# Kernel optimization log

Measured on AMD Instinct MI355X. Metric: run time of the kernel, lower is better.

The kernel has to match this reference:

```python
import jax, jax.numpy as jnp
import numpy as np

B, S, H, D = 256, 512, 512, 1  # batch, seq_len, rnn_hid_size (== S*D), input_dim


def lstm_cell(x, h, c, Wih, Whh, bih, bhh):
    # torch.nn.LSTMCell: gates ordered i, f, g, o
    g = x @ Wih.T + bih + h @ Whh.T + bhh  # [B, 4H]
    i, f, gg, o = jnp.split(g, 4, axis=-1)
    i = jax.nn.sigmoid(i)
    f = jax.nn.sigmoid(f)
    gg = jnp.tanh(gg)
    o = jax.nn.sigmoid(o)
    c_new = f * c + i * gg
    h_new = o * jnp.tanh(c_new)
    return h_new, c_new


def setup_inputs() -> dict:
    key = jax.random.key(0)
    ks = jax.random.split(key, 14)
    sc = 1.0 / np.sqrt(H)  # torch LSTMCell/Linear default uniform bound
    u = lambda k, shape: jax.random.uniform(k, shape, jnp.float32, -sc, sc)
    values = jax.random.normal(ks[0], (B, S), jnp.float32)
    masks = jax.random.randint(ks[1], (B, S), 0, 2).astype(jnp.float32)
    return {
        "values": values,
        "masks": masks,
        "Wih_f": u(ks[2], (4 * H, D)), "Whh_f": u(ks[3], (4 * H, H)),
        "bih_f": u(ks[4], (4 * H,)), "bhh_f": u(ks[5], (4 * H,)),
        "Wih_b": u(ks[6], (4 * H, D)), "Whh_b": u(ks[7], (4 * H, H)),
        "bih_b": u(ks[8], (4 * H,)), "bhh_b": u(ks[9], (4 * H,)),
        "W_imp": u(ks[10], (D, H)), "b_imp": u(ks[11], (D,)),
    }


def reference(values, masks, Wih_f, Whh_f, bih_f, bhh_f,
              Wih_b, Whh_b, bih_b, bhh_b, W_imp, b_imp):
    x_f = values[:, :, None]  # [B, S, 1]
    m_f = masks[:, :, None]
    # flip over axis 2 (size 1) is a no-op, matching the original exactly
    x_b = jnp.flip(x_f, axis=2)
    m_b = jnp.flip(m_f, axis=2)

    start_f = jnp.full((B, D), 128.0, jnp.float32)
    start_b = jnp.full((B, D), -128.0, jnp.float32)
    z = jnp.zeros((B, H), jnp.float32)
    h_f, c_f = lstm_cell(start_f, z, z, Wih_f, Whh_f, bih_f, bhh_f)
    h_b, c_b = lstm_cell(start_b, z, z, Wih_b, Whh_b, bih_b, bhh_b)

    xs = (jnp.swapaxes(x_f, 0, 1), jnp.swapaxes(m_f, 0, 1),
          jnp.swapaxes(x_b, 0, 1), jnp.swapaxes(m_b, 0, 1))  # [S, B, 1] each

    def step(carry, inp):
        hf, cf, hb, cb = carry
        xf, mf, xb, mb = inp
        imp_f = hf @ W_imp.T + b_imp
        imp_b = hb @ W_imp.T + b_imp
        cc_f = (1.0 - mf) * xf + mf * imp_f
        cc_b = (1.0 - mb) * xb + mb * imp_b
        hf, cf = lstm_cell(cc_f, hf, cf, Wih_f, Whh_f, bih_f, bhh_f)
        hb, cb = lstm_cell(cc_b, hb, cb, Wih_b, Whh_b, bih_b, bhh_b)
        return (hf, cf, hb, cb), None

    (h_f, c_f, h_b, c_b), _ = jax.lax.scan(step, (h_f, c_f, h_b, c_b), xs)
    h = h_f + h_b  # [B, H]
    imputations = h.reshape(B, S, D)  # requires H == S * D
    out = imputations * (1.0 - m_f) + x_f * m_f
    return h, out
```

## Files before the change

kernel.cpp:

```cpp
#include <hip/hip_runtime.h>
#include <stdint.h>

#define B_ 256
#define S_ 512
#define H_ 512

#define XM_STRIDE 513
#define LDS_BYTES 56320

typedef __attribute__((ext_vector_type(4))) float f32x4;
typedef __attribute__((ext_vector_type(4))) int   i32x4;
typedef __attribute__((ext_vector_type(8))) short s16x8;

__device__ __forceinline__ short f2bf(float f) {
    union { float f; uint32_t u; } c; c.f = f;
    uint32_t u = c.u;
    u += 0x7fffu + ((u >> 16) & 1u);
    return (short)(u >> 16);
}
__device__ __forceinline__ float bflo(uint32_t u) { return __builtin_bit_cast(float, u << 16); }
__device__ __forceinline__ float bfhi(uint32_t u) { return __builtin_bit_cast(float, u & 0xffff0000u); }
__device__ __forceinline__ float sig_(float x)  { return 1.0f / (1.0f + __expf(-x)); }
__device__ __forceinline__ float tanh_(float x) { return 1.0f - 2.0f / (1.0f + __expf(2.0f * x)); }

__device__ __forceinline__ void load_a16_issue(const void* p, i32x4* a) {
    asm volatile(
        "global_load_dwordx4 %0, %16, off sc0 sc1\n\t"
        "global_load_dwordx4 %1, %16, off offset:64 sc0 sc1\n\t"
        "global_load_dwordx4 %2, %16, off offset:128 sc0 sc1\n\t"
        "global_load_dwordx4 %3, %16, off offset:192 sc0 sc1\n\t"
        "global_load_dwordx4 %4, %16, off offset:256 sc0 sc1\n\t"
        "global_load_dwordx4 %5, %16, off offset:320 sc0 sc1\n\t"
        "global_load_dwordx4 %6, %16, off offset:384 sc0 sc1\n\t"
        "global_load_dwordx4 %7, %16, off offset:448 sc0 sc1\n\t"
        "global_load_dwordx4 %8, %16, off offset:512 sc0 sc1\n\t"
        "global_load_dwordx4 %9, %16, off offset:576 sc0 sc1\n\t"
        "global_load_dwordx4 %10, %16, off offset:640 sc0 sc1\n\t"
        "global_load_dwordx4 %11, %16, off offset:704 sc0 sc1\n\t"
        "global_load_dwordx4 %12, %16, off offset:768 sc0 sc1\n\t"
        "global_load_dwordx4 %13, %16, off offset:832 sc0 sc1\n\t"
        "global_load_dwordx4 %14, %16, off offset:896 sc0 sc1\n\t"
        "global_load_dwordx4 %15, %16, off offset:960 sc0 sc1"
        : "=v"(a[0]), "=v"(a[1]), "=v"(a[2]), "=v"(a[3]),
          "=v"(a[4]), "=v"(a[5]), "=v"(a[6]), "=v"(a[7]),
          "=v"(a[8]), "=v"(a[9]), "=v"(a[10]), "=v"(a[11]),
          "=v"(a[12]), "=v"(a[13]), "=v"(a[14]), "=v"(a[15])
        : "v"(p)
        : "memory");
}
#define AWAIT(imm, x0, x1, x2, x3) \
    asm volatile("s_waitcnt vmcnt(" #imm ")" : "+v"(x0), "+v"(x1), "+v"(x2), "+v"(x3) :: "memory")

__device__ __forceinline__ void store_h4(void* p, int h0, int h1, int h2, int h3) {
    asm volatile(
        "global_store_short %4, %0, off sc0 sc1\n\t"
        "global_store_short %4, %1, off offset:1024 sc0 sc1\n\t"
        "global_store_short %4, %2, off offset:2048 sc0 sc1\n\t"
        "global_store_short %4, %3, off offset:3072 sc0 sc1"
        :: "v"(h0), "v"(h1), "v"(h2), "v"(h3), "v"(p)
        : "memory");
}

__global__ void __launch_bounds__(128, 1)
lstm_kernel(const float* __restrict__ values, const float* __restrict__ masks,
            const float* __restrict__ Wih_f, const float* __restrict__ Whh_f,
            const float* __restrict__ bih_f, const float* __restrict__ bhh_f,
            const float* __restrict__ Wih_b, const float* __restrict__ Whh_b,
            const float* __restrict__ bih_b, const float* __restrict__ bhh_b,
            const float* __restrict__ W_imp, const float* __restrict__ b_imp,
            unsigned int* ctrs, short* h_buf, float* hfin)
{
    extern __shared__ char smem_raw[];
    short*    imp_lds = (short*)smem_raw;
    uint32_t* xm_lds  = (uint32_t*)(smem_raw + 16384);

    uint32_t* flags = (uint32_t*)ctrs + 64;

    const int tid  = threadIdx.x;
    const int lane = tid & 63;
    const int wave = tid >> 6;
    const int nw = wave;

    const int bid = blockIdx.x;
    const int g   = bid & 15;
    const int w   = (bid >> 4) & 15;
    const int d   = bid >> 8;
    const int cluster = d * 16 + g;

    const float* Whh = d ? Whh_b : Whh_f;
    const float* Wih = d ? Wih_b : Wih_f;
    const float* bih = d ? bih_b : bih_f;
    const float* bhh = d ? bhh_b : bhh_f;

    const int col16 = lane & 15;
    const int koff4 = lane >> 4;
    const int jcol  = w * 32 + nw * 16 + col16;

    for (int c = tid; c < 1024; c += 128) {
        int ckoff = (c >> 4) & 3, ckb = c >> 6;
        int k0 = ckb * 32 + ckoff * 8;
        short* dst = &imp_lds[c * 8];
        #pragma unroll
        for (int j = 0; j < 8; ++j) dst[j] = f2bf(W_imp[k0 + j]);
    }
    for (int i = tid; i < 16 * 512; i += 128) {
        int r = i >> 9, s = i & 511;
        float x = values[(g * 16 + r) * S_ + s];
        float m = masks[(g * 16 + r) * S_ + s];
        float a = x * (1.0f - m);
        xm_lds[r * XM_STRIDE + s] =
            (uint32_t)(uint16_t)f2bf(a) | ((uint32_t)(uint16_t)f2bf(m) << 16);
    }

    s16x8 bfr[4][16];
    {
        const float* base = Whh + (size_t)jcol * 512 + koff4 * 8;
        #pragma unroll
        for (int gg = 0; gg < 4; ++gg) {
            const float* src = base + (size_t)gg * 512 * 512;
            #pragma unroll
            for (int kb = 0; kb < 16; ++kb) {
                f32x4 v0 = *(const f32x4*)(src + kb * 32);
                f32x4 v1 = *(const f32x4*)(src + kb * 32 + 4);
                s16x8 b;
                b[0] = f2bf(v0[0]); b[1] = f2bf(v0[1]); b[2] = f2bf(v0[2]); b[3] = f2bf(v0[3]);
                b[4] = f2bf(v1[0]); b[5] = f2bf(v1[1]); b[6] = f2bf(v1[2]); b[7] = f2bf(v1[3]);
                bfr[gg][kb] = b;
            }
        }
    }

    float bias[4], wih[4];
    #pragma unroll
    for (int gg = 0; gg < 4; ++gg) {
        int gc = gg * 512 + jcol;
        bias[gg] = bih[gc] + bhh[gc];
        wih[gg]  = Wih[gc];
    }
    const float bimp  = b_imp[0];
    const float start = d ? -128.0f : 128.0f;

    const int arow    = g * 16 + col16;
    const int rowloc  = koff4 * 4;
    const int rowbase = g * 16 + rowloc;
    const int imp_off = (koff4 * 16 + col16) * 8;

    uint32_t*       myflag = flags + cluster * 16 + w;
    const uint32_t* pollp  = flags + cluster * 16 + col16;

    __syncthreads();

    float c_reg[4];
    {
        float pre[4];
        #pragma unroll
        for (int gg = 0; gg < 4; ++gg) pre[gg] = start * wih[gg] + bias[gg];
        float i0 = sig_(pre[0]), g0 = tanh_(pre[2]), o0 = sig_(pre[3]);
        float c0 = i0 * g0;
        float h0 = o0 * tanh_(c0);
        #pragma unroll
        for (int r = 0; r < 4; ++r) c_reg[r] = c0;
        int hb16 = (int)(unsigned short)(unsigned)f2bf(h0);
        short* dst = h_buf + d * (B_ * H_) + (size_t)rowbase * H_ + jcol;
        store_h4(dst, hb16, hb16, hb16, hb16);
    }
    asm volatile("s_waitcnt vmcnt(0)" ::: "memory");
    __syncthreads();
    if (tid == 0)
        asm volatile("global_store_dword %0, %1, off sc0 sc1" :: "v"(myflag), "v"(1u) : "memory");

    for (int t = 0; t < S_; ++t) {
        const int p = t & 1;
        const short* hb_r = h_buf + p       * (2 * B_ * H_) + d * (B_ * H_);
        short*       hb_w = h_buf + (p ^ 1) * (2 * B_ * H_) + d * (B_ * H_);

        if (wave == 0) {
            const uint32_t tgt = (uint32_t)(t + 1);
            for (;;) {
                uint32_t f;
                asm volatile("global_load_dword %0, %1, off sc0 sc1\n\ts_waitcnt vmcnt(0)"
                             : "=v"(f) : "v"(pollp) : "memory");
                if (__ballot(f >= tgt) == ~0ull) break;
                __builtin_amdgcn_s_sleep(2);
            }
        }
        __syncthreads();

        i32x4 a_regs[16];
        load_a16_issue(hb_r + (size_t)arow * H_ + koff4 * 8, a_regs);

        f32x4 acc0 = {0,0,0,0}, acc1 = {0,0,0,0}, acc2 = {0,0,0,0}, acc3 = {0,0,0,0};
        f32x4 acc4 = {0,0,0,0};
        AWAIT(12, a_regs[0], a_regs[1], a_regs[2], a_regs[3]);
        #pragma unroll
        for (int kb = 0; kb < 4; ++kb) {
            s16x8 a = __builtin_bit_cast(s16x8, a_regs[kb]);
            acc0 = __builtin_amdgcn_mfma_f32_16x16x32_bf16(a, bfr[0][kb], acc0, 0, 0, 0);
            acc1 = __builtin_amdgcn_mfma_f32_16x16x32_bf16(a, bfr[1][kb], acc1, 0, 0, 0);
            acc2 = __builtin_amdgcn_mfma_f32_16x16x32_bf16(a, bfr[2][kb], acc2, 0, 0, 0);
            acc3 = __builtin_amdgcn_mfma_f32_16x16x32_bf16(a, bfr[3][kb], acc3, 0, 0, 0);
            s16x8 b4 = *(const s16x8*)&imp_lds[kb * 512 + imp_off];
            acc4 = __builtin_amdgcn_mfma_f32_16x16x32_bf16(a, b4, acc4, 0, 0, 0);
        }
        AWAIT(8, a_regs[4], a_regs[5], a_regs[6], a_regs[7]);
        #pragma unroll
        for (int kb = 4; kb < 8; ++kb) {
            s16x8 a = __builtin_bit_cast(s16x8, a_regs[kb]);
            acc0 = __builtin_amdgcn_mfma_f32_16x16x32_bf16(a, bfr[0][kb], acc0, 0, 0, 0);
            acc1 = __builtin_amdgcn_mfma_f32_16x16x32_bf16(a, bfr[1][kb], acc1, 0, 0, 0);
            acc2 = __builtin_amdgcn_mfma_f32_16x16x32_bf16(a, bfr[2][kb], acc2, 0, 0, 0);
            acc3 = __builtin_amdgcn_mfma_f32_16x16x32_bf16(a, bfr[3][kb], acc3, 0, 0, 0);
            s16x8 b4 = *(const s16x8*)&imp_lds[kb * 512 + imp_off];
            acc4 = __builtin_amdgcn_mfma_f32_16x16x32_bf16(a, b4, acc4, 0, 0, 0);
        }
        AWAIT(4, a_regs[8], a_regs[9], a_regs[10], a_regs[11]);
        #pragma unroll
        for (int kb = 8; kb < 12; ++kb) {
            s16x8 a = __builtin_bit_cast(s16x8, a_regs[kb]);
            acc0 = __builtin_amdgcn_mfma_f32_16x16x32_bf16(a, bfr[0][kb], acc0, 0, 0, 0);
            acc1 = __builtin_amdgcn_mfma_f32_16x16x32_bf16(a, bfr[1][kb], acc1, 0, 0, 0);
            acc2 = __builtin_amdgcn_mfma_f32_16x16x32_bf16(a, bfr[2][kb], acc2, 0, 0, 0);
            acc3 = __builtin_amdgcn_mfma_f32_16x16x32_bf16(a, bfr[3][kb], acc3, 0, 0, 0);
            s16x8 b4 = *(const s16x8*)&imp_lds[kb * 512 + imp_off];
            acc4 = __builtin_amdgcn_mfma_f32_16x16x32_bf16(a, b4, acc4, 0, 0, 0);
        }
        AWAIT(0, a_regs[12], a_regs[13], a_regs[14], a_regs[15]);
        #pragma unroll
        for (int kb = 12; kb < 16; ++kb) {
            s16x8 a = __builtin_bit_cast(s16x8, a_regs[kb]);
            acc0 = __builtin_amdgcn_mfma_f32_16x16x32_bf16(a, bfr[0][kb], acc0, 0, 0, 0);
            acc1 = __builtin_amdgcn_mfma_f32_16x16x32_bf16(a, bfr[1][kb], acc1, 0, 0, 0);
            acc2 = __builtin_amdgcn_mfma_f32_16x16x32_bf16(a, bfr[2][kb], acc2, 0, 0, 0);
            acc3 = __builtin_amdgcn_mfma_f32_16x16x32_bf16(a, bfr[3][kb], acc3, 0, 0, 0);
            s16x8 b4 = *(const s16x8*)&imp_lds[kb * 512 + imp_off];
            acc4 = __builtin_amdgcn_mfma_f32_16x16x32_bf16(a, b4, acc4, 0, 0, 0);
        }

        int hbits[4];
        #pragma unroll
        for (int r = 0; r < 4; ++r) {
            uint32_t pk = xm_lds[(rowloc + r) * XM_STRIDE + t];
            float cc = bflo(pk) + bfhi(pk) * (acc4[r] + bimp);
            float pi = acc0[r] + cc * wih[0] + bias[0];
            float pf = acc1[r] + cc * wih[1] + bias[1];
            float pg = acc2[r] + cc * wih[2] + bias[2];
            float po = acc3[r] + cc * wih[3] + bias[3];
            float iv = sig_(pi), fv = sig_(pf), gv = tanh_(pg), ov = sig_(po);
            c_reg[r] = fv * c_reg[r] + iv * gv;
            float hn = ov * tanh_(c_reg[r]);
            hbits[r] = (int)(unsigned short)(unsigned)f2bf(hn);
            if (t == S_ - 1) hfin[d * (B_ * H_) + (rowbase + r) * H_ + jcol] = hn;
        }
        store_h4(hb_w + (size_t)rowbase * H_ + jcol, hbits[0], hbits[1], hbits[2], hbits[3]);

        asm volatile("s_waitcnt vmcnt(0)" ::: "memory");
        __syncthreads();
        if (tid == 0)
            asm volatile("global_store_dword %0, %1, off sc0 sc1"
                         :: "v"(myflag), "v"((uint32_t)(t + 2)) : "memory");
    }
}

__global__ void __launch_bounds__(256)
epilogue_kernel(const float* __restrict__ values, const float* __restrict__ masks,
                const float* __restrict__ hfin, float* __restrict__ out)
{
    int i = blockIdx.x * 256 + threadIdx.x;
    float h = hfin[i] + hfin[B_ * H_ + i];
    out[i] = h;
    float xv = values[i], mv = masks[i];
    out[B_ * H_ + i] = h * (1.0f - mv) + xv * mv;
}

extern "C" void kernel_launch(void* const* d_in, const int* in_sizes, int n_in,
                              void* d_out, int out_size, void* d_ws, size_t ws_size,
                              hipStream_t stream) {
    const float* values = (const float*)d_in[0];
    const float* masks  = (const float*)d_in[1];
    const float* Wih_f  = (const float*)d_in[2];
    const float* Whh_f  = (const float*)d_in[3];
    const float* bih_f  = (const float*)d_in[4];
    const float* bhh_f  = (const float*)d_in[5];
    const float* Wih_b  = (const float*)d_in[6];
    const float* Whh_b  = (const float*)d_in[7];
    const float* bih_b  = (const float*)d_in[8];
    const float* bhh_b  = (const float*)d_in[9];
    const float* W_imp  = (const float*)d_in[10];
    const float* b_imp  = (const float*)d_in[11];

    unsigned int* ctrs = (unsigned int*)d_ws;
    short* h_buf = (short*)((char*)d_ws + 8192);
    float* hfin  = (float*)((char*)d_ws + 8192 + 2 * 2 * B_ * H_ * sizeof(short));

    hipMemsetAsync(d_ws, 0, 8192, stream);

    hipFuncSetAttribute((const void*)lstm_kernel,
                        hipFuncAttributeMaxDynamicSharedMemorySize, LDS_BYTES);

    void* args[] = {
        (void*)&values, (void*)&masks,
        (void*)&Wih_f, (void*)&Whh_f, (void*)&bih_f, (void*)&bhh_f,
        (void*)&Wih_b, (void*)&Whh_b, (void*)&bih_b, (void*)&bhh_b,
        (void*)&W_imp, (void*)&b_imp,
        (void*)&ctrs, (void*)&h_buf, (void*)&hfin
    };
    hipError_t err = hipLaunchCooperativeKernel((const void*)lstm_kernel,
                                                dim3(512), dim3(128), args,
                                                (unsigned int)LDS_BYTES, stream);
    if (err != hipSuccess) {
        lstm_kernel<<<dim3(512), dim3(128), LDS_BYTES, stream>>>(
            values, masks, Wih_f, Whh_f, bih_f, bhh_f,
            Wih_b, Whh_b, bih_b, bhh_b, W_imp, b_imp, ctrs, h_buf, hfin);
    }

    epilogue_kernel<<<dim3((B_ * H_) / 256), dim3(256), 0, stream>>>(
        values, masks, hfin, (float*)d_out);
}
```

Before: 2.342 ms.

## Replace flag-based barrier with step-tagged h values, widen blocks to 256 threads

Drops the per-cluster flag counters. Each bf16 h value is now packed into a 32-bit word with the timestep in its upper half, and readers spin on the data itself until every tag matches, so the separate flag store, its vmcnt wait and the extra syncthreads per step are gone. Blocks grow to four waves covering 64 columns, and the grid halves to 256 blocks. Each wave loads a quarter of the h row slice and shares it through a swizzled LDS buffer before the MFMAs. The cost is twice the h_buf traffic, a larger memset of the workspace, and hfin now being written into the output buffer before the epilogue reads it back.

```diff
diff --git a/kernel.cpp b/kernel.cpp
--- a/kernel.cpp
+++ b/kernel.cpp
@@ -6,7 +6,7 @@
 #define H_ 512
 
 #define XM_STRIDE 513
-#define LDS_BYTES 56320
+#define LDS_BYTES 81984
 
 typedef __attribute__((ext_vector_type(4))) float f32x4;
 typedef __attribute__((ext_vector_type(4))) int   i32x4;
@@ -23,69 +23,63 @@
 __device__ __forceinline__ float sig_(float x)  { return 1.0f / (1.0f + __expf(-x)); }
 __device__ __forceinline__ float tanh_(float x) { return 1.0f - 2.0f / (1.0f + __expf(2.0f * x)); }
 
-__device__ __forceinline__ void load_a16_issue(const void* p, i32x4* a) {
+__device__ __forceinline__ uint32_t pklo(uint32_t hi, uint32_t lo) {
+    return __builtin_amdgcn_perm(hi, lo, 0x05040100u);
+}
+
+__device__ __forceinline__ void load_a8_issue(const void* p, i32x4* a) {
     asm volatile(
-        "global_load_dwordx4 %0, %16, off sc0 sc1\n\t"
-        "global_load_dwordx4 %1, %16, off offset:64 sc0 sc1\n\t"
-        "global_load_dwordx4 %2, %16, off offset:128 sc0 sc1\n\t"
-        "global_load_dwordx4 %3, %16, off offset:192 sc0 sc1\n\t"
-        "global_load_dwordx4 %4, %16, off offset:256 sc0 sc1\n\t"
-        "global_load_dwordx4 %5, %16, off offset:320 sc0 sc1\n\t"
-        "global_load_dwordx4 %6, %16, off offset:384 sc0 sc1\n\t"
-        "global_load_dwordx4 %7, %16, off offset:448 sc0 sc1\n\t"
-        "global_load_dwordx4 %8, %16, off offset:512 sc0 sc1\n\t"
-        "global_load_dwordx4 %9, %16, off offset:576 sc0 sc1\n\t"
-        "global_load_dwordx4 %10, %16, off offset:640 sc0 sc1\n\t"
-        "global_load_dwordx4 %11, %16, off offset:704 sc0 sc1\n\t"
-        "global_load_dwordx4 %12, %16, off offset:768 sc0 sc1\n\t"
-        "global_load_dwordx4 %13, %16, off offset:832 sc0 sc1\n\t"
-        "global_load_dwordx4 %14, %16, off offset:896 sc0 sc1\n\t"
-        "global_load_dwordx4 %15, %16, off offset:960 sc0 sc1"
-        : "=v"(a[0]), "=v"(a[1]), "=v"(a[2]), "=v"(a[3]),
-          "=v"(a[4]), "=v"(a[5]), "=v"(a[6]), "=v"(a[7]),
-          "=v"(a[8]), "=v"(a[9]), "=v"(a[10]), "=v"(a[11]),
-          "=v"(a[12]), "=v"(a[13]), "=v"(a[14]), "=v"(a[15])
+        "global_load_dwordx4 %0, %8, off sc0 sc1\n\t"
+        "global_load_dwordx4 %1, %8, off offset:16 sc0 sc1\n\t"
+        "global_load_dwordx4 %2, %8, off offset:128 sc0 sc1\n\t"
+        "global_load_dwordx4 %3, %8, off offset:144 sc0 sc1\n\t"
+        "global_load_dwordx4 %4, %8, off offset:256 sc0 sc1\n\t"
+        "global_load_dwordx4 %5, %8, off offset:272 sc0 sc1\n\t"
+        "global_load_dwordx4 %6, %8, off offset:384 sc0 sc1\n\t"
+        "global_load_dwordx4 %7, %8, off offset:400 sc0 sc1"
+        : "=&v"(a[0]), "=&v"(a[1]), "=&v"(a[2]), "=&v"(a[3]),
+          "=&v"(a[4]), "=&v"(a[5]), "=&v"(a[6]), "=&v"(a[7])
         : "v"(p)
         : "memory");
 }
-#define AWAIT(imm, x0, x1, x2, x3) \
-    asm volatile("s_waitcnt vmcnt(" #imm ")" : "+v"(x0), "+v"(x1), "+v"(x2), "+v"(x3) :: "memory")
-
-__device__ __forceinline__ void store_h4(void* p, int h0, int h1, int h2, int h3) {
+#define AWAIT8(a) \
+    asm volatile("s_waitcnt vmcnt(0)" \
+        : "+v"(a[0]), "+v"(a[1]), "+v"(a[2]), "+v"(a[3]), \
+          "+v"(a[4]), "+v"(a[5]), "+v"(a[6]), "+v"(a[7]) :: "memory")
+
+__device__ __forceinline__ void store_h4d(void* p, uint32_t d0, uint32_t d1,
+                                          uint32_t d2, uint32_t d3) {
     asm volatile(
-        "global_store_short %4, %0, off sc0 sc1\n\t"
-        "global_store_short %4, %1, off offset:1024 sc0 sc1\n\t"
-        "global_store_short %4, %2, off offset:2048 sc0 sc1\n\t"
-        "global_store_short %4, %3, off offset:3072 sc0 sc1"
-        :: "v"(h0), "v"(h1), "v"(h2), "v"(h3), "v"(p)
+        "global_store_dword %4, %0, off offset:-4096 sc0 sc1\n\t"
+        "global_store_dword %4, %1, off offset:-2048 sc0 sc1\n\t"
+        "global_store_dword %4, %2, off sc0 sc1\n\t"
+        "global_store_dword %4, %3, off offset:2048 sc0 sc1"
+        :: "v"(d0), "v"(d1), "v"(d2), "v"(d3), "v"(p)
         : "memory");
 }
 
-__global__ void __launch_bounds__(128, 1)
+__global__ void __launch_bounds__(256, 1)
 lstm_kernel(const float* __restrict__ values, const float* __restrict__ masks,
             const float* __restrict__ Wih_f, const float* __restrict__ Whh_f,
             const float* __restrict__ bih_f, const float* __restrict__ bhh_f,
             const float* __restrict__ Wih_b, const float* __restrict__ Whh_b,
             const float* __restrict__ bih_b, const float* __restrict__ bhh_b,
             const float* __restrict__ W_imp, const float* __restrict__ b_imp,
-            unsigned int* ctrs, short* h_buf, float* hfin)
+            uint32_t* h_buf, float* hfin)
 {
     extern __shared__ char smem_raw[];
     short*    imp_lds = (short*)smem_raw;
     uint32_t* xm_lds  = (uint32_t*)(smem_raw + 16384);
-
-    uint32_t* flags = (uint32_t*)ctrs + 64;
+    char*     aP      = smem_raw + 49216;
 
     const int tid  = threadIdx.x;
     const int lane = tid & 63;
-    const int wave = tid >> 6;
-    const int nw = wave;
+    const int nw   = tid >> 6;
 
     const int bid = blockIdx.x;
     const int g   = bid & 15;
-    const int w   = (bid >> 4) & 15;
-    const int d   = bid >> 8;
-    const int cluster = d * 16 + g;
+    const int w   = (bid >> 4) & 7;
+    const int d   = bid >> 7;
 
     const float* Whh = d ? Whh_b : Whh_f;
     const float* Wih = d ? Wih_b : Wih_f;
@@ -94,16 +88,17 @@
 
     const int col16 = lane & 15;
     const int koff4 = lane >> 4;
-    const int jcol  = w * 32 + nw * 16 + col16;
-
-    for (int c = tid; c < 1024; c += 128) {
+    const int jcol  = w * 64 + nw * 16 + col16;
+    const int swz   = (col16 & 7) << 4;
+
+    for (int c = tid; c < 1024; c += 256) {
         int ckoff = (c >> 4) & 3, ckb = c >> 6;
         int k0 = ckb * 32 + ckoff * 8;
         short* dst = &imp_lds[c * 8];
         #pragma unroll
         for (int j = 0; j < 8; ++j) dst[j] = f2bf(W_imp[k0 + j]);
     }
-    for (int i = tid; i < 16 * 512; i += 128) {
+    for (int i = tid; i < 16 * 512; i += 256) {
         int r = i >> 9, s = i & 511;
         float x = values[(g * 16 + r) * S_ + s];
         float m = masks[(g * 16 + r) * S_ + s];
@@ -145,11 +140,6 @@
     const int rowbase = g * 16 + rowloc;
     const int imp_off = (koff4 * 16 + col16) * 8;
 
-    uint32_t*       myflag = flags + cluster * 16 + w;
-    const uint32_t* pollp  = flags + cluster * 16 + col16;
-
-    __syncthreads();
-
     float c_reg[4];
     {
         float pre[4];
@@ -160,41 +150,61 @@
         float h0 = o0 * tanh_(c0);
         #pragma unroll
         for (int r = 0; r < 4; ++r) c_reg[r] = c0;
-        int hb16 = (int)(unsigned short)(unsigned)f2bf(h0);
-        short* dst = h_buf + d * (B_ * H_) + (size_t)rowbase * H_ + jcol;
-        store_h4(dst, hb16, hb16, hb16, hb16);
-    }
-    asm volatile("s_waitcnt vmcnt(0)" ::: "memory");
+        uint32_t dwi = (1u << 16) | (uint32_t)(unsigned short)(unsigned)f2bf(h0);
+        uint32_t* dst = h_buf + (size_t)d * (B_ * H_)
+                        + (size_t)(rowbase + 2) * H_ + jcol;
+        store_h4d(dst, dwi, dwi, dwi, dwi);
+    }
+
     __syncthreads();
-    if (tid == 0)
-        asm volatile("global_store_dword %0, %1, off sc0 sc1" :: "v"(myflag), "v"(1u) : "memory");
 
     for (int t = 0; t < S_; ++t) {
         const int p = t & 1;
-        const short* hb_r = h_buf + p       * (2 * B_ * H_) + d * (B_ * H_);
-        short*       hb_w = h_buf + (p ^ 1) * (2 * B_ * H_) + d * (B_ * H_);
-
-        if (wave == 0) {
-            const uint32_t tgt = (uint32_t)(t + 1);
-            for (;;) {
-                uint32_t f;
-                asm volatile("global_load_dword %0, %1, off sc0 sc1\n\ts_waitcnt vmcnt(0)"
-                             : "=v"(f) : "v"(pollp) : "memory");
-                if (__ballot(f >= tgt) == ~0ull) break;
-                __builtin_amdgcn_s_sleep(2);
+        const uint32_t* hb_r = h_buf + (size_t)p       * (2 * B_ * H_) + (size_t)d * (B_ * H_);
+        uint32_t*       hb_w = h_buf + (size_t)(p ^ 1) * (2 * B_ * H_) + (size_t)d * (B_ * H_);
+
+        const uint32_t tgtv = (uint32_t)(t + 1) << 16;
+        const uint32_t* ap = hb_r + (size_t)arow * H_ + nw * 128 + koff4 * 8;
+        i32x4 araw[8];
+        load_a8_issue(ap, araw);
+        for (;;) {
+            AWAIT8(araw);
+            uint32_t mn = 0xffffffffu;
+            #pragma unroll
+            for (int j = 0; j < 8; ++j) {
+                uint32_t u0 = (uint32_t)araw[j][0], u1 = (uint32_t)araw[j][1];
+                uint32_t u2 = (uint32_t)araw[j][2], u3 = (uint32_t)araw[j][3];
+                uint32_t m0 = u0 < u1 ? u0 : u1;
+                uint32_t m1 = u2 < u3 ? u2 : u3;
+                uint32_t mm = m0 < m1 ? m0 : m1;
+                mn = mn < mm ? mn : mm;
             }
+            if (__ballot(mn >= tgtv) == ~0ull) break;
+            __builtin_amdgcn_s_sleep(2);
+            load_a8_issue(ap, araw);
+        }
+
+        {
+            char* wb = aP + p * 16384 + col16 * 1024;
+            #pragma unroll
+            for (int j = 0; j < 4; ++j) {
+                i32x4 pk;
+                pk[0] = (int)pklo((uint32_t)araw[2*j  ][1], (uint32_t)araw[2*j  ][0]);
+                pk[1] = (int)pklo((uint32_t)araw[2*j  ][3], (uint32_t)araw[2*j  ][2]);
+                pk[2] = (int)pklo((uint32_t)araw[2*j+1][1], (uint32_t)araw[2*j+1][0]);
+                pk[3] = (int)pklo((uint32_t)araw[2*j+1][3], (uint32_t)araw[2*j+1][2]);
+                int boff = (((nw * 4 + j) * 64 + koff4 * 16) ^ swz);
+                *(i32x4*)(wb + boff) = pk;
+            }
         }
         __syncthreads();
-
-        i32x4 a_regs[16];
-        load_a16_issue(hb_r + (size_t)arow * H_ + koff4 * 8, a_regs);
 
         f32x4 acc0 = {0,0,0,0}, acc1 = {0,0,0,0}, acc2 = {0,0,0,0}, acc3 = {0,0,0,0};
         f32x4 acc4 = {0,0,0,0};
-        AWAIT(12, a_regs[0], a_regs[1], a_regs[2], a_regs[3]);
-        #pragma unroll
-        for (int kb = 0; kb < 4; ++kb) {
-            s16x8 a = __builtin_bit_cast(s16x8, a_regs[kb]);
+        const char* rb = aP + p * 16384 + col16 * 1024;
+        #pragma unroll
+        for (int kb = 0; kb < 16; ++kb) {
+            s16x8 a = *(const s16x8*)(rb + ((kb * 64 + koff4 * 16) ^ swz));
             acc0 = __builtin_amdgcn_mfma_f32_16x16x32_bf16(a, bfr[0][kb], acc0, 0, 0, 0);
             acc1 = __builtin_amdgcn_mfma_f32_16x16x32_bf16(a, bfr[1][kb], acc1, 0, 0, 0);
             acc2 = __builtin_amdgcn_mfma_f32_16x16x32_bf16(a, bfr[2][kb], acc2, 0, 0, 0);
@@ -202,41 +212,9 @@
             s16x8 b4 = *(const s16x8*)&imp_lds[kb * 512 + imp_off];
             acc4 = __builtin_amdgcn_mfma_f32_16x16x32_bf16(a, b4, acc4, 0, 0, 0);
         }
-        AWAIT(8, a_regs[4], a_regs[5], a_regs[6], a_regs[7]);
-        #pragma unroll
-        for (int kb = 4; kb < 8; ++kb) {
-            s16x8 a = __builtin_bit_cast(s16x8, a_regs[kb]);
-            acc0 = __builtin_amdgcn_mfma_f32_16x16x32_bf16(a, bfr[0][kb], acc0, 0, 0, 0);
-            acc1 = __builtin_amdgcn_mfma_f32_16x16x32_bf16(a, bfr[1][kb], acc1, 0, 0, 0);
-            acc2 = __builtin_amdgcn_mfma_f32_16x16x32_bf16(a, bfr[2][kb], acc2, 0, 0, 0);
-            acc3 = __builtin_amdgcn_mfma_f32_16x16x32_bf16(a, bfr[3][kb], acc3, 0, 0, 0);
-            s16x8 b4 = *(const s16x8*)&imp_lds[kb * 512 + imp_off];
-            acc4 = __builtin_amdgcn_mfma_f32_16x16x32_bf16(a, b4, acc4, 0, 0, 0);
-        }
-        AWAIT(4, a_regs[8], a_regs[9], a_regs[10], a_regs[11]);
-        #pragma unroll
-        for (int kb = 8; kb < 12; ++kb) {
-            s16x8 a = __builtin_bit_cast(s16x8, a_regs[kb]);
-            acc0 = __builtin_amdgcn_mfma_f32_16x16x32_bf16(a, bfr[0][kb], acc0, 0, 0, 0);
-            acc1 = __builtin_amdgcn_mfma_f32_16x16x32_bf16(a, bfr[1][kb], acc1, 0, 0, 0);
-            acc2 = __builtin_amdgcn_mfma_f32_16x16x32_bf16(a, bfr[2][kb], acc2, 0, 0, 0);
-            acc3 = __builtin_amdgcn_mfma_f32_16x16x32_bf16(a, bfr[3][kb], acc3, 0, 0, 0);
-            s16x8 b4 = *(const s16x8*)&imp_lds[kb * 512 + imp_off];
-            acc4 = __builtin_amdgcn_mfma_f32_16x16x32_bf16(a, b4, acc4, 0, 0, 0);
-        }
-        AWAIT(0, a_regs[12], a_regs[13], a_regs[14], a_regs[15]);
-        #pragma unroll
-        for (int kb = 12; kb < 16; ++kb) {
-            s16x8 a = __builtin_bit_cast(s16x8, a_regs[kb]);
-            acc0 = __builtin_amdgcn_mfma_f32_16x16x32_bf16(a, bfr[0][kb], acc0, 0, 0, 0);
-            acc1 = __builtin_amdgcn_mfma_f32_16x16x32_bf16(a, bfr[1][kb], acc1, 0, 0, 0);
-            acc2 = __builtin_amdgcn_mfma_f32_16x16x32_bf16(a, bfr[2][kb], acc2, 0, 0, 0);
-            acc3 = __builtin_amdgcn_mfma_f32_16x16x32_bf16(a, bfr[3][kb], acc3, 0, 0, 0);
-            s16x8 b4 = *(const s16x8*)&imp_lds[kb * 512 + imp_off];
-            acc4 = __builtin_amdgcn_mfma_f32_16x16x32_bf16(a, b4, acc4, 0, 0, 0);
-        }
-
-        int hbits[4];
+
+        const uint32_t tagw = (uint32_t)(t + 2) << 16;
+        uint32_t dw[4];
         #pragma unroll
         for (int r = 0; r < 4; ++r) {
             uint32_t pk = xm_lds[(rowloc + r) * XM_STRIDE + t];
@@ -248,16 +226,10 @@
             float iv = sig_(pi), fv = sig_(pf), gv = tanh_(pg), ov = sig_(po);
             c_reg[r] = fv * c_reg[r] + iv * gv;
             float hn = ov * tanh_(c_reg[r]);
-            hbits[r] = (int)(unsigned short)(unsigned)f2bf(hn);
+            dw[r] = tagw | (uint32_t)(unsigned short)(unsigned)f2bf(hn);
             if (t == S_ - 1) hfin[d * (B_ * H_) + (rowbase + r) * H_ + jcol] = hn;
         }
-        store_h4(hb_w + (size_t)rowbase * H_ + jcol, hbits[0], hbits[1], hbits[2], hbits[3]);
-
-        asm volatile("s_waitcnt vmcnt(0)" ::: "memory");
-        __syncthreads();
-        if (tid == 0)
-            asm volatile("global_store_dword %0, %1, off sc0 sc1"
-                         :: "v"(myflag), "v"((uint32_t)(t + 2)) : "memory");
+        store_h4d(hb_w + (size_t)(rowbase + 2) * H_ + jcol, dw[0], dw[1], dw[2], dw[3]);
     }
 }
 
@@ -267,9 +239,10 @@
 {
     int i = blockIdx.x * 256 + threadIdx.x;
     float h = hfin[i] + hfin[B_ * H_ + i];
+    float xv = values[i], mv = masks[i];
+    float blend = h * (1.0f - mv) + xv * mv;
     out[i] = h;
-    float xv = values[i], mv = masks[i];
-    out[B_ * H_ + i] = h * (1.0f - mv) + xv * mv;
+    out[B_ * H_ + i] = blend;
 }
 
 extern "C" void kernel_launch(void* const* d_in, const int* in_sizes, int n_in,
@@ -288,11 +261,10 @@
     const float* W_imp  = (const float*)d_in[10];
     const float* b_imp  = (const float*)d_in[11];
 
-    unsigned int* ctrs = (unsigned int*)d_ws;
-    short* h_buf = (short*)((char*)d_ws + 8192);
-    float* hfin  = (float*)((char*)d_ws + 8192 + 2 * 2 * B_ * H_ * sizeof(short));
-
-    hipMemsetAsync(d_ws, 0, 8192, stream);
+    uint32_t* h_buf = (uint32_t*)d_ws;
+    float*    hfin  = (float*)d_out;
+
+    hipMemsetAsync(d_ws, 0, (size_t)2 * 2 * B_ * H_ * 4, stream);
 
     hipFuncSetAttribute((const void*)lstm_kernel,
                         hipFuncAttributeMaxDynamicSharedMemorySize, LDS_BYTES);
@@ -302,15 +274,15 @@
         (void*)&Wih_f, (void*)&Whh_f, (void*)&bih_f, (void*)&bhh_f,
         (void*)&Wih_b, (void*)&Whh_b, (void*)&bih_b, (void*)&bhh_b,
         (void*)&W_imp, (void*)&b_imp,
-        (void*)&ctrs, (void*)&h_buf, (void*)&hfin
+        (void*)&h_buf, (void*)&hfin
     };
     hipError_t err = hipLaunchCooperativeKernel((const void*)lstm_kernel,
-                                                dim3(512), dim3(128), args,
+                                                dim3(256), dim3(256), args,
                                                 (unsigned int)LDS_BYTES, stream);
     if (err != hipSuccess) {
-        lstm_kernel<<<dim3(512), dim3(128), LDS_BYTES, stream>>>(
+        lstm_kernel<<<dim3(256), dim3(256), LDS_BYTES, stream>>>(
             values, masks, Wih_f, Whh_f, bih_f, bhh_f,
-            Wih_b, Whh_b, bih_b, bhh_b, W_imp, b_imp, ctrs, h_buf, hfin);
+            Wih_b, Whh_b, bih_b, bhh_b, W_imp, b_imp, h_buf, hfin);
     }
 
     epilogue_kernel<<<dim3((B_ * H_) / 256), dim3(256), 0, stream>>>(
```

New measurement: 2.936 ms. 25.4% more time.

## Co-locate LSTM clusters per XCD and use L2-scope loads when all peers share an XCC

Applied to the files above, without the earlier changes.

Block indices are remapped so that each 16-block cluster (one direction and batch group) is meant to land on a single XCD under round-robin dispatch. Each block publishes its hardware XCC id in the upper bits of its progress flag. If every peer reports the same XCC, polling and hidden-state loads switch from system-coherent (sc0 sc1) to L2-scope (sc0) accesses, which avoids bypassing the shared L2 on the per-step recurrence. It falls back to the old coherent path when placement differs, at the cost of one extra startup handshake and reliance on the dispatcher's XCD assignment.

```diff
diff --git a/kernel.cpp b/kernel.cpp
--- a/kernel.cpp
+++ b/kernel.cpp
@@ -48,6 +48,31 @@
         : "v"(p)
         : "memory");
 }
+__device__ __forceinline__ void load_a16_issue_l2(const void* p, i32x4* a) {
+    asm volatile(
+        "global_load_dwordx4 %0, %16, off sc0\n\t"
+        "global_load_dwordx4 %1, %16, off offset:64 sc0\n\t"
+        "global_load_dwordx4 %2, %16, off offset:128 sc0\n\t"
+        "global_load_dwordx4 %3, %16, off offset:192 sc0\n\t"
+        "global_load_dwordx4 %4, %16, off offset:256 sc0\n\t"
+        "global_load_dwordx4 %5, %16, off offset:320 sc0\n\t"
+        "global_load_dwordx4 %6, %16, off offset:384 sc0\n\t"
+        "global_load_dwordx4 %7, %16, off offset:448 sc0\n\t"
+        "global_load_dwordx4 %8, %16, off offset:512 sc0\n\t"
+        "global_load_dwordx4 %9, %16, off offset:576 sc0\n\t"
+        "global_load_dwordx4 %10, %16, off offset:640 sc0\n\t"
+        "global_load_dwordx4 %11, %16, off offset:704 sc0\n\t"
+        "global_load_dwordx4 %12, %16, off offset:768 sc0\n\t"
+        "global_load_dwordx4 %13, %16, off offset:832 sc0\n\t"
+        "global_load_dwordx4 %14, %16, off offset:896 sc0\n\t"
+        "global_load_dwordx4 %15, %16, off offset:960 sc0"
+        : "=v"(a[0]), "=v"(a[1]), "=v"(a[2]), "=v"(a[3]),
+          "=v"(a[4]), "=v"(a[5]), "=v"(a[6]), "=v"(a[7]),
+          "=v"(a[8]), "=v"(a[9]), "=v"(a[10]), "=v"(a[11]),
+          "=v"(a[12]), "=v"(a[13]), "=v"(a[14]), "=v"(a[15])
+        : "v"(p)
+        : "memory");
+}
 #define AWAIT(imm, x0, x1, x2, x3) \
     asm volatile("s_waitcnt vmcnt(" #imm ")" : "+v"(x0), "+v"(x1), "+v"(x2), "+v"(x3) :: "memory")
 
@@ -71,8 +96,9 @@
             unsigned int* ctrs, short* h_buf, float* hfin)
 {
     extern __shared__ char smem_raw[];
-    short*    imp_lds = (short*)smem_raw;
-    uint32_t* xm_lds  = (uint32_t*)(smem_raw + 16384);
+    short*        imp_lds  = (short*)smem_raw;
+    uint32_t*     xm_lds   = (uint32_t*)(smem_raw + 16384);
+    volatile int* mode_lds = (volatile int*)(smem_raw + 49216);
 
     uint32_t* flags = (uint32_t*)ctrs + 64;
 
@@ -82,10 +108,12 @@
     const int nw = wave;
 
     const int bid = blockIdx.x;
-    const int g   = bid & 15;
-    const int w   = (bid >> 4) & 15;
-    const int d   = bid >> 8;
-    const int cluster = d * 16 + g;
+    const int xcd = bid & 7;
+    const int q   = bid >> 3;
+    const int w   = q >> 2;
+    const int cluster = xcd * 4 + (q & 3);
+    const int d   = cluster >> 4;
+    const int g   = cluster & 15;
 
     const float* Whh = d ? Whh_b : Whh_f;
     const float* Wih = d ? Wih_b : Wih_f;
@@ -95,6 +123,10 @@
     const int col16 = lane & 15;
     const int koff4 = lane >> 4;
     const int jcol  = w * 32 + nw * 16 + col16;
+
+    uint32_t xcc;
+    asm volatile("s_getreg_b32 %0, hwreg(HW_REG_XCC_ID)" : "=s"(xcc));
+    xcc &= 0xfu;
 
     for (int c = tid; c < 1024; c += 128) {
         int ckoff = (c >> 4) & 3, ckb = c >> 6;
@@ -167,7 +199,22 @@
     asm volatile("s_waitcnt vmcnt(0)" ::: "memory");
     __syncthreads();
     if (tid == 0)
-        asm volatile("global_store_dword %0, %1, off sc0 sc1" :: "v"(myflag), "v"(1u) : "memory");
+        asm volatile("global_store_dword %0, %1, off sc0 sc1"
+                     :: "v"(myflag), "v"((xcc << 16) | 1u) : "memory");
+
+    if (wave == 0) {
+        uint32_t f;
+        for (;;) {
+            asm volatile("global_load_dword %0, %1, off sc0 sc1\n\ts_waitcnt vmcnt(0)"
+                         : "=v"(f) : "v"(pollp) : "memory");
+            if (__ballot((f & 0xffffu) >= 1u) == ~0ull) break;
+            __builtin_amdgcn_s_sleep(2);
+        }
+        if (lane == 0)
+            *mode_lds = (__ballot((f >> 16) == xcc) == ~0ull) ? 1 : 0;
+    }
+    __syncthreads();
+    const int fastu = __builtin_amdgcn_readfirstlane(*mode_lds);
 
     for (int t = 0; t < S_; ++t) {
         const int p = t & 1;
@@ -176,18 +223,30 @@
 
         if (wave == 0) {
             const uint32_t tgt = (uint32_t)(t + 1);
-            for (;;) {
-                uint32_t f;
-                asm volatile("global_load_dword %0, %1, off sc0 sc1\n\ts_waitcnt vmcnt(0)"
-                             : "=v"(f) : "v"(pollp) : "memory");
-                if (__ballot(f >= tgt) == ~0ull) break;
-                __builtin_amdgcn_s_sleep(2);
+            if (fastu) {
+                for (;;) {
+                    uint32_t f;
+                    asm volatile("global_load_dword %0, %1, off sc0\n\ts_waitcnt vmcnt(0)"
+                                 : "=v"(f) : "v"(pollp) : "memory");
+                    if (__ballot((f & 0xffffu) >= tgt) == ~0ull) break;
+                    __builtin_amdgcn_s_sleep(2);
+                }
+            } else {
+                for (;;) {
+                    uint32_t f;
+                    asm volatile("global_load_dword %0, %1, off sc0 sc1\n\ts_waitcnt vmcnt(0)"
+                                 : "=v"(f) : "v"(pollp) : "memory");
+                    if (__ballot((f & 0xffffu) >= tgt) == ~0ull) break;
+                    __builtin_amdgcn_s_sleep(2);
+                }
             }
         }
         __syncthreads();
 
         i32x4 a_regs[16];
-        load_a16_issue(hb_r + (size_t)arow * H_ + koff4 * 8, a_regs);
+        const short* ap = hb_r + (size_t)arow * H_ + koff4 * 8;
+        if (fastu) load_a16_issue_l2(ap, a_regs);
+        else       load_a16_issue(ap, a_regs);
 
         f32x4 acc0 = {0,0,0,0}, acc1 = {0,0,0,0}, acc2 = {0,0,0,0}, acc3 = {0,0,0,0};
         f32x4 acc4 = {0,0,0,0};
@@ -257,7 +316,7 @@
         __syncthreads();
         if (tid == 0)
             asm volatile("global_store_dword %0, %1, off sc0 sc1"
-                         :: "v"(myflag), "v"((uint32_t)(t + 2)) : "memory");
+                         :: "v"(myflag), "v"((xcc << 16) | (uint32_t)(t + 2)) : "memory");
     }
 }
 
```

Measured after the change: 3.102 ms. 32.5% more time.
